# Performance work log

Measured on AMD Instinct MI355X. Metric: run time of the kernel, lower is better.

Reference implementation:

```python
import jax, jax.numpy as jnp
import numpy as np

PATCH = 16
CH = 3


def setup_inputs() -> dict:
    key = jax.random.key(0)
    k1, k2, k3 = jax.random.split(key, 3)
    B, H = 16, 512
    embed_dim = PATCH * PATCH * CH  # 768
    x = jax.random.normal(k1, (B, CH, H, H), dtype=jnp.float32)
    fan_in = CH * PATCH * PATCH
    w = jax.random.normal(k2, (embed_dim, CH, PATCH, PATCH), dtype=jnp.float32) / np.float32(np.sqrt(fan_in))
    b = jax.random.normal(k3, (embed_dim,), dtype=jnp.float32) * 0.01
    return {"x": x, "w": w, "b": b}


def reference(x, w, b):
    p = w.shape[2]                      # patch_size
    B, C, imgsize, _ = x.shape
    pn = imgsize // p                   # patch_num (NOTE: pre-padding count, as in source)
    # zero-pad by one patch on every side
    xp = jnp.pad(x, ((0, 0), (0, 0), (p, p), (p, p)))
    # strided patch-embed conv: [B, embed_dim, pn+2, pn+2]
    xt = jax.lax.conv_general_dilated(xp, w, window_strides=(p, p), padding='VALID')
    xt = xt + b[None, :, None, None]
    B1, C1, H1, W1 = xt.shape           # H1 = W1 = pn + 2
    xt = xt.reshape(B1, C1, H1 * W1)
    # same (buggy-looking but faithful) index set / stride-pn neighbors as the source
    idxs = jnp.array([i * pn + j for i in range(1, pn - 1) for j in range(1, pn)], dtype=jnp.int32)
    inv8 = jnp.float32(1.0 / 8.0)

    def body(buf, idx):
        # torch aliases x_final=x_temp, so reads see earlier in-place writes -> sequential scan
        s = (buf[:, :, idx - pn] + buf[:, :, idx + pn]
             + buf[:, :, idx - 1] + buf[:, :, idx + 1]
             + buf[:, :, idx - pn - 1] + buf[:, :, idx - pn + 1]
             + buf[:, :, idx + pn - 1] + buf[:, :, idx + pn + 1]) * inv8
        return buf.at[:, :, idx].set(s), None

    xf, _ = jax.lax.scan(body, xt, idxs)
    side = imgsize + 2 * p              # embed_dim*H1*W1 == C*side*side by construction
    out = xf.reshape(B1, C, side, side)
    return out[:, :, p:imgsize + p, p:imgsize + p]
```

## Files before the change

kernel.cpp:

```cpp
#include <hip/hip_runtime.h>
#include <hip/hip_bf16.h>


typedef __attribute__((ext_vector_type(8))) short s8v;
typedef __attribute__((ext_vector_type(4))) float f4v;
typedef __attribute__((ext_vector_type(8))) unsigned short us8;
typedef __attribute__((ext_vector_type(4))) unsigned short us4;

__device__ __forceinline__ unsigned short f2bf(float f) {
    __hip_bfloat16 h = __float2bfloat16(f);
    return *reinterpret_cast<unsigned short*>(&h);
}
__device__ __forceinline__ float bf2f(unsigned short u) {
    union { unsigned int i; float f; } c; c.i = (unsigned int)u << 16; return c.f;
}

__global__ __launch_bounds__(256) void prep_w_k(const float* __restrict__ w,
                                                unsigned short* __restrict__ w_bf) {
    int g = blockIdx.x * 256 + threadIdx.x;
    int f = g << 3;
    const float4 v0 = *(const float4*)(w + f);
    const float4 v1 = *(const float4*)(w + f + 4);
    us8 u;
    u[0] = f2bf(v0.x); u[1] = f2bf(v0.y); u[2] = f2bf(v0.z); u[3] = f2bf(v0.w);
    u[4] = f2bf(v1.x); u[5] = f2bf(v1.y); u[6] = f2bf(v1.z); u[7] = f2bf(v1.w);
    *(us8*)(w_bf + f) = u;
}

__global__ __launch_bounds__(512, 4) void conv_gemm_rs_k(const float* __restrict__ x,
                                                         const unsigned short* __restrict__ W,
                                                         const float* __restrict__ bias,
                                                         unsigned short* __restrict__ xt) {
    __shared__ __align__(16) unsigned short As[2][128 * 32];
    __shared__ __align__(16) unsigned short Bs[2][192 * 32];
    const int tid  = threadIdx.x;
    const int lane = tid & 63, wv = tid >> 6;
    const int wr = wv >> 2, wc = wv & 3;
    const int m0 = blockIdx.x << 7;
    const int n0 = blockIdx.y * 192;
    const int bb = m0 >> 10;
    const int ph0 = (m0 >> 5) & 31;

    const int arow = tid >> 2, ach = tid & 3;
    const int phl  = arow >> 5, pw = arow & 31;
    const int aoff = (arow << 5) + ((ach ^ ((arow >> 1) & 3)) << 3);
    const float* xbase = x + (size_t)bb * 786432 + (ph0 + phl) * 8192
                           + (ach >> 1) * 512 + (pw << 4) + ((ach & 1) << 3);

    const int brow = tid >> 1, bpair = tid & 1;
    const int bxr  = (brow >> 1) & 3;
    const int boff0 = (brow << 5) + ((((bpair << 1))     ^ bxr) << 3);
    const int boff1 = (brow << 5) + ((((bpair << 1) | 1) ^ bxr) << 3);
    const unsigned short* wbase = W + (size_t)(n0 + brow) * 768 + (bpair << 4);

    float4 xr_[2][2];
    us8    wf_[2][2];

    auto gload = [&](int s, int t) {
        const float* sp = xbase + (t >> 3) * 262144 + (t & 7) * 1024;
        xr_[s][0] = *(const float4*)(sp);
        xr_[s][1] = *(const float4*)(sp + 4);
        if (tid < 384) {
            const unsigned short* ws = wbase + (t << 5);
            wf_[s][0] = *(const us8*)(ws);
            wf_[s][1] = *(const us8*)(ws + 8);
        }
    };
    auto store = [&](int s, int buf) {
        us8 lo;
        lo[0]=f2bf(xr_[s][0].x); lo[1]=f2bf(xr_[s][0].y);
        lo[2]=f2bf(xr_[s][0].z); lo[3]=f2bf(xr_[s][0].w);
        lo[4]=f2bf(xr_[s][1].x); lo[5]=f2bf(xr_[s][1].y);
        lo[6]=f2bf(xr_[s][1].z); lo[7]=f2bf(xr_[s][1].w);
        *(us8*)(As[buf] + aoff) = lo;
        if (tid < 384) {
            *(us8*)(Bs[buf] + boff0) = wf_[s][0];
            *(us8*)(Bs[buf] + boff1) = wf_[s][1];
        }
    };

    f4v acc[4][3] = {};
    gload(0, 0);
    store(0, 0);
    __syncthreads();

    const int cq = lane >> 4, l15 = lane & 15;
    #pragma unroll
    for (int t = 0; t < 24; ++t) {
        const int p = t & 1;
        if (t < 23) gload(p ^ 1, t + 1);
        s8v a[4], b[3];
        #pragma unroll
        for (int mi = 0; mi < 4; ++mi) {
            int ra = (wr << 6) + (mi << 4) + l15;
            a[mi] = *(const s8v*)(As[p] + (ra << 5) + ((cq ^ ((ra >> 1) & 3)) << 3));
        }
        #pragma unroll
        for (int ni = 0; ni < 3; ++ni) {
            int rb = wc * 48 + (ni << 4) + l15;
            b[ni] = *(const s8v*)(Bs[p] + (rb << 5) + ((cq ^ ((rb >> 1) & 3)) << 3));
        }
        #pragma unroll
        for (int mi = 0; mi < 4; ++mi)
            #pragma unroll
            for (int ni = 0; ni < 3; ++ni)
                acc[mi][ni] = __builtin_amdgcn_mfma_f32_16x16x32_bf16(a[mi], b[ni], acc[mi][ni], 0, 0, 0);
        if (t < 23) store(p ^ 1, p ^ 1);
        __syncthreads();
    }

    #pragma unroll
    for (int mi = 0; mi < 4; ++mi) {
        int m  = m0 + (wr << 6) + (mi << 4) + (cq << 2);
        int ph = (m >> 5) & 31, pwm = m & 31;
        unsigned short* dst = xt + (((size_t)bb * 768) << 10) + (ph << 5) + pwm;
        #pragma unroll
        for (int ni = 0; ni < 3; ++ni) {
            int n = n0 + wc * 48 + (ni << 4) + l15;
            float bv = bias[n];
            us4 o;
            o[0] = f2bf(acc[mi][ni][0] + bv);
            o[1] = f2bf(acc[mi][ni][1] + bv);
            o[2] = f2bf(acc[mi][ni][2] + bv);
            o[3] = f2bf(acc[mi][ni][3] + bv);
            *(us4*)(dst + ((size_t)n << 10)) = o;
        }
    }
}

__global__ __launch_bounds__(256) void scan_emit_k(const unsigned short* __restrict__ xt,
                                                   const float* __restrict__ bias,
                                                   float* __restrict__ out) {
    const int grp = (blockIdx.x * 256 + threadIdx.x) >> 5;
    const int j   = threadIdx.x & 31;
    const int b   = grp / 768;
    const int c1  = grp - b * 768;
    const unsigned short* basep = xt + ((size_t)grp << 10);
    float* outb = out + (size_t)b * 786432;
    const int fl0 = c1 * 1156;
    const float bias_c = bias[c1];

    auto emit = [&](int fl, float v) {
        unsigned int c   = (fl >= 591872) ? 2u : (fl >= 295936 ? 1u : 0u);
        unsigned int rem = (unsigned int)fl - c * 295936u;
        unsigned int y   = rem / 544u;
        unsigned int xx  = rem - y * 544u;
        if (y >= 16u && y < 528u && xx >= 16u && xx < 528u)
            outb[(size_t)c * 262144 + (y - 16) * 512 + (xx - 16)] = v;
    };
    auto sel = [&](int p) -> float {
        unsigned int h = (unsigned int)p / 34u;
        unsigned int w = (unsigned int)p - h * 34u;
        if ((h == 0u) | (h == 33u) | (w == 0u) | (w == 33u)) return bias_c;
        return bf2f(basep[(h - 1u) * 32u + (w - 1u)]);
    };

    float co = sel( 32 + j);
    float no = sel( 64 + j);
    float o2 = sel( 96 + j);
    float o3 = sel(128 + j);
    emit(fl0 + j, bias_c);
    float pn   = bias_c;
    float po_h = bias_c;

    for (int i = 1; i <= 30; ++i) {
        float ld = sel((i + 4) * 32 + j);
        float co_head = __shfl(co, 0, 32);
        float no_head = __shfl(no, 0, 32);
        float n2_head = __shfl(o2, 0, 32);
        float UL = __shfl_up(pn, 1, 32);   if (j == 1)  UL = po_h;
        float U  = pn;
        float UR = __shfl_down(pn, 1, 32); if (j == 31) UR = co_head;
        float Rr = __shfl_down(co, 1, 32); if (j == 31) Rr = no_head;
        float D1 = __shfl_up(no, 1, 32);
        float D2 = no;
        float D3 = __shfl_down(no, 1, 32); if (j == 31) D3 = n2_head;
        float bv = (((UL + U) + (UR + Rr)) + ((D1 + D2) + D3)) * 0.125f;
        if (j == 1) bv += co_head * 0.125f;
        float t;
        t = __shfl_up(bv, 1, 32);  bv += (j > 1) ? 0.125f * t : 0.f;
        t = __shfl_up(bv, 2, 32);  bv += (j > 2) ? 0.015625f * t : 0.f;
        t = __shfl_up(bv, 4, 32);  bv += (j > 4) ? 2.44140625e-4f * t : 0.f;
        emit(fl0 + i * 32 + j, (j == 0) ? co : bv);
        pn   = bv;
        po_h = co_head;
        co = no; no = o2; o2 = o3; o3 = ld;
    }
    emit(fl0 +  992 + j, co);
    emit(fl0 + 1024 + j, no);
    emit(fl0 + 1056 + j, o2);
    emit(fl0 + 1088 + j, o3);
    emit(fl0 + 1120 + j, sel(1120 + j));
    if (j < 4) emit(fl0 + 1152 + j, bias_c);
}

extern "C" void kernel_launch(void* const* d_in, const int* in_sizes, int n_in,
                              void* d_out, int out_size, void* d_ws, size_t ws_size,
                              hipStream_t stream) {
    const float* x    = (const float*)d_in[0];
    const float* w    = (const float*)d_in[1];
    const float* bias = (const float*)d_in[2];
    float* out = (float*)d_out;
    unsigned short* xt = (unsigned short*)d_ws;

    unsigned short* w_bf = (unsigned short*)d_out;

    prep_w_k<<<288, 256, 0, stream>>>(w, w_bf);
    conv_gemm_rs_k<<<dim3(128, 4), 512, 0, stream>>>(x, w_bf, bias, xt);
    scan_emit_k<<<1536, 256, 0, stream>>>(xt, bias, out);
}
```

Measured before the change: 74.73 us.

## Load GEMM weight fragments directly to registers; incremental output indexing in scan

The GEMM kernel stops staging the bf16 weight tile through shared memory. Each lane now loads its B fragments straight from global memory into double-buffered registers, which removes the B shared-memory writes and reads and shrinks LDS use. The cost is that weight fragments are duplicated across the waves that share a column group, so global or L2 traffic rises and register pressure grows. Separately, the scan kernel replaces the per-element divide-and-mod output index math with an incrementally updated row/column counter.

Result: slower. 93.06 us (+24.5%).

```diff
diff --git a/kernel.cpp b/kernel.cpp
--- a/kernel.cpp
+++ b/kernel.cpp
@@ -32,7 +32,6 @@
                                                          const float* __restrict__ bias,
                                                          unsigned short* __restrict__ xt) {
     __shared__ __align__(16) unsigned short As[2][128 * 32];
-    __shared__ __align__(16) unsigned short Bs[2][192 * 32];
     const int tid  = threadIdx.x;
     const int lane = tid & 63, wv = tid >> 6;
     const int wr = wv >> 2, wc = wv & 3;
@@ -40,6 +39,7 @@
     const int n0 = blockIdx.y * 192;
     const int bb = m0 >> 10;
     const int ph0 = (m0 >> 5) & 31;
+    const int cq = lane >> 4, l15 = lane & 15;
 
     const int arow = tid >> 2, ach = tid & 3;
     const int phl  = arow >> 5, pw = arow & 31;
@@ -47,65 +47,55 @@
     const float* xbase = x + (size_t)bb * 786432 + (ph0 + phl) * 8192
                            + (ach >> 1) * 512 + (pw << 4) + ((ach & 1) << 3);
 
-    const int brow = tid >> 1, bpair = tid & 1;
-    const int bxr  = (brow >> 1) & 3;
-    const int boff0 = (brow << 5) + ((((bpair << 1))     ^ bxr) << 3);
-    const int boff1 = (brow << 5) + ((((bpair << 1) | 1) ^ bxr) << 3);
-    const unsigned short* wbase = W + (size_t)(n0 + brow) * 768 + (bpair << 4);
+    const unsigned short* wfrag[3];
+    #pragma unroll
+    for (int ni = 0; ni < 3; ++ni)
+        wfrag[ni] = W + (size_t)(n0 + wc * 48 + (ni << 4) + l15) * 768 + (cq << 3);
 
     float4 xr_[2][2];
-    us8    wf_[2][2];
-
-    auto gload = [&](int s, int t) {
+    s8v    bfr_[2][3];
+
+    auto gloadA = [&](int s, int t) {
         const float* sp = xbase + (t >> 3) * 262144 + (t & 7) * 1024;
         xr_[s][0] = *(const float4*)(sp);
         xr_[s][1] = *(const float4*)(sp + 4);
-        if (tid < 384) {
-            const unsigned short* ws = wbase + (t << 5);
-            wf_[s][0] = *(const us8*)(ws);
-            wf_[s][1] = *(const us8*)(ws + 8);
-        }
-    };
-    auto store = [&](int s, int buf) {
+    };
+    auto gloadB = [&](int s, int t) {
+        #pragma unroll
+        for (int ni = 0; ni < 3; ++ni)
+            bfr_[s][ni] = *(const s8v*)(wfrag[ni] + (t << 5));
+    };
+    auto storeA = [&](int s, int buf) {
         us8 lo;
         lo[0]=f2bf(xr_[s][0].x); lo[1]=f2bf(xr_[s][0].y);
         lo[2]=f2bf(xr_[s][0].z); lo[3]=f2bf(xr_[s][0].w);
         lo[4]=f2bf(xr_[s][1].x); lo[5]=f2bf(xr_[s][1].y);
         lo[6]=f2bf(xr_[s][1].z); lo[7]=f2bf(xr_[s][1].w);
         *(us8*)(As[buf] + aoff) = lo;
-        if (tid < 384) {
-            *(us8*)(Bs[buf] + boff0) = wf_[s][0];
-            *(us8*)(Bs[buf] + boff1) = wf_[s][1];
-        }
     };
 
     f4v acc[4][3] = {};
-    gload(0, 0);
-    store(0, 0);
+    gloadA(0, 0);
+    gloadB(0, 0);
+    storeA(0, 0);
     __syncthreads();
 
-    const int cq = lane >> 4, l15 = lane & 15;
     #pragma unroll
     for (int t = 0; t < 24; ++t) {
         const int p = t & 1;
-        if (t < 23) gload(p ^ 1, t + 1);
-        s8v a[4], b[3];
+        if (t < 23) { gloadA(p ^ 1, t + 1); gloadB(p ^ 1, t + 1); }
+        s8v a[4];
         #pragma unroll
         for (int mi = 0; mi < 4; ++mi) {
             int ra = (wr << 6) + (mi << 4) + l15;
             a[mi] = *(const s8v*)(As[p] + (ra << 5) + ((cq ^ ((ra >> 1) & 3)) << 3));
         }
         #pragma unroll
-        for (int ni = 0; ni < 3; ++ni) {
-            int rb = wc * 48 + (ni << 4) + l15;
-            b[ni] = *(const s8v*)(Bs[p] + (rb << 5) + ((cq ^ ((rb >> 1) & 3)) << 3));
-        }
-        #pragma unroll
         for (int mi = 0; mi < 4; ++mi)
             #pragma unroll
             for (int ni = 0; ni < 3; ++ni)
-                acc[mi][ni] = __builtin_amdgcn_mfma_f32_16x16x32_bf16(a[mi], b[ni], acc[mi][ni], 0, 0, 0);
-        if (t < 23) store(p ^ 1, p ^ 1);
+                acc[mi][ni] = __builtin_amdgcn_mfma_f32_16x16x32_bf16(a[mi], bfr_[p][ni], acc[mi][ni], 0, 0, 0);
+        if (t < 23) storeA(p ^ 1, p ^ 1);
         __syncthreads();
     }
 
@@ -136,17 +126,22 @@
     const int b   = grp / 768;
     const int c1  = grp - b * 768;
     const unsigned short* basep = xt + ((size_t)grp << 10);
-    float* outb = out + (size_t)b * 786432;
-    const int fl0 = c1 * 1156;
     const float bias_c = bias[c1];
-
-    auto emit = [&](int fl, float v) {
-        unsigned int c   = (fl >= 591872) ? 2u : (fl >= 295936 ? 1u : 0u);
-        unsigned int rem = (unsigned int)fl - c * 295936u;
-        unsigned int y   = rem / 544u;
-        unsigned int xx  = rem - y * 544u;
-        if (y >= 16u && y < 528u && xx >= 16u && xx < 528u)
-            outb[(size_t)c * 262144 + (y - 16) * 512 + (xx - 16)] = v;
+    float* baseo = out + (size_t)b * 786432 + (size_t)(c1 >> 8) * 262144;
+
+    int rem = (c1 & 255) * 1156 + j;
+    int ey  = rem / 544;
+    int ex  = rem - ey * 544;
+    int eo  = (ey - 16) * 512 + (ex - 16);
+
+    auto estep = [&](float v) {
+        if (((unsigned)(ex - 16) < 512u) & ((unsigned)(ey - 16) < 512u))
+            baseo[eo] = v;
+        ex += 32;
+        int wrp = (ex >= 544);
+        ex -= wrp ? 544 : 0;
+        ey += wrp;
+        eo += wrp ? 0 : 32;
     };
     auto sel = [&](int p) -> float {
         unsigned int h = (unsigned int)p / 34u;
@@ -159,7 +154,7 @@
     float no = sel( 64 + j);
     float o2 = sel( 96 + j);
     float o3 = sel(128 + j);
-    emit(fl0 + j, bias_c);
+    estep(bias_c);
     float pn   = bias_c;
     float po_h = bias_c;
 
@@ -181,17 +176,17 @@
         t = __shfl_up(bv, 1, 32);  bv += (j > 1) ? 0.125f * t : 0.f;
         t = __shfl_up(bv, 2, 32);  bv += (j > 2) ? 0.015625f * t : 0.f;
         t = __shfl_up(bv, 4, 32);  bv += (j > 4) ? 2.44140625e-4f * t : 0.f;
-        emit(fl0 + i * 32 + j, (j == 0) ? co : bv);
+        estep((j == 0) ? co : bv);
         pn   = bv;
         po_h = co_head;
         co = no; no = o2; o2 = o3; o3 = ld;
     }
-    emit(fl0 +  992 + j, co);
-    emit(fl0 + 1024 + j, no);
-    emit(fl0 + 1056 + j, o2);
-    emit(fl0 + 1088 + j, o3);
-    emit(fl0 + 1120 + j, sel(1120 + j));
-    if (j < 4) emit(fl0 + 1152 + j, bias_c);
+    estep(co);
+    estep(no);
+    estep(o2);
+    estep(o3);
+    estep(sel(1120 + j));
+    if (j < 4) estep(bias_c);
 }
 
 extern "C" void kernel_launch(void* const* d_in, const int* in_sizes, int n_in,
```
